# Kernel tuning notes

Measured on AMD Instinct MI355X. Metric: run time of the kernel, lower is better.

## Reference

```python
import jax, jax.numpy as jnp
import numpy as np

B = 512        # batch
TW = 45        # raw wav token length
C = 512        # n_embd
H = 8          # heads
L = 8          # decoder layers
V = 1000       # wav vocab
NLAB = 5       # label vocab
HID = 2048     # 4*C mlp hidden
OH = 768       # output head hidden
WIN, TRAIN = 30, 44
LN_EPS = 1e-5


def _build_mask(t):
    # triangular (strict upper) + sliding-window lower band, tiled 3x3 over segments
    m = np.triu(np.ones((TRAIN, TRAIN), dtype=bool), 1)
    for i in range(WIN, TRAIN):
        m[i, : i - WIN + 1] = True
    m = m[:t, :t]
    return jnp.asarray(np.tile(m, (3, 3)))  # [3t, 3t], True = masked


def setup_inputs() -> dict:
    key = jax.random.key(0)
    ks = iter(jax.random.split(key, 64))

    def rn(shape, s=0.02):
        return jax.random.normal(next(ks), shape, jnp.float32) * s

    inp = {
        'label': jax.random.randint(next(ks), (B, 1), 0, NLAB),
        'wav1': jax.random.randint(next(ks), (B, TW), 0, V),
        'wav2': jax.random.randint(next(ks), (B, TW), 0, V),
        # embeddings
        'emb_label': rn((NLAB, C), 1.0),
        'emb_w1': rn((V, C), 1.0),
        'emb_w2': rn((V, C), 1.0),
        # per-layer stacked params (leading dim L) for lax.scan
        'ln1_g': jnp.ones((L, 3, C), jnp.float32),
        'ln1_b': jnp.zeros((L, 3, C), jnp.float32),
        'ln2_g': jnp.ones((L, 3, C), jnp.float32),
        'ln2_b': jnp.zeros((L, 3, C), jnp.float32),
        'Wq': rn((L, C, C)), 'bq': jnp.zeros((L, C), jnp.float32),
        'Wk': rn((L, C, C)), 'bk': jnp.zeros((L, C), jnp.float32),
        'Wv': rn((L, C, C)), 'bv': jnp.zeros((L, C), jnp.float32),
        'Wp': rn((L, C, C)), 'bp': jnp.zeros((L, C), jnp.float32),
        'W1': rn((L, C, HID)), 'b1': jnp.zeros((L, HID), jnp.float32),
        'W2': rn((L, HID, C)), 'b2': jnp.zeros((L, C), jnp.float32),
        # output heads
        'o1W1': rn((C, OH)), 'o1b1': jnp.zeros((OH,), jnp.float32),
        'o1W2': rn((OH, V)), 'o1b2': jnp.zeros((V,), jnp.float32),
        'o2W1': rn((C, OH)), 'o2b1': jnp.zeros((OH,), jnp.float32),
        'o2W2': rn((OH, V)), 'o2b2': jnp.zeros((V,), jnp.float32),
    }
    return inp


def _forward(label, wav1, wav2, emb_label, emb_w1, emb_w2,
             ln1_g, ln1_b, ln2_g, ln2_b, Wq, bq, Wk, bk, Wv, bv, Wp, bp,
             W1, b1, W2, b2, o1W1, o1b1, o1W2, o1b2, o2W1, o2b1, o2W2, o2b2):
    wav1_src, wav1_tgt = wav1[:, :-1], wav1[:, 1:]
    wav2_src, wav2_tgt = wav2[:, :-1], wav2[:, 1:]
    b, t = wav1_src.shape
    label_rep = jnp.broadcast_to(label, (b, t))

    feat = jnp.concatenate([emb_label[label_rep], emb_w1[wav1_src], emb_w2[wav2_src]], axis=1)  # [B,3t,C]
    mask = _build_mask(t)  # [3t,3t] bool
    hd = C // H

    def ln3(x, g, be):
        # three separate LayerNorms over the 3 equal segments
        xr = x.reshape(b, 3, t, C)
        mu = xr.mean(-1, keepdims=True)
        var = xr.var(-1, keepdims=True)
        xn = (xr - mu) * jax.lax.rsqrt(var + LN_EPS)
        return (xn * g[None, :, None, :] + be[None, :, None, :]).reshape(b, 3 * t, C)

    def layer(x, p):
        g1, be1, g2, be2, wq, bq_, wk, bk_, wv, bv_, wp, bp_, w1, b1_, w2, b2_ = p
        h = ln3(x, g1, be1)
        q = (h @ wq + bq_).reshape(b, 3 * t, H, hd).transpose(0, 2, 1, 3)
        k = (h @ wk + bk_).reshape(b, 3 * t, H, hd).transpose(0, 2, 1, 3)
        v = (h @ wv + bv_).reshape(b, 3 * t, H, hd).transpose(0, 2, 1, 3)
        att = jnp.einsum('bhqd,bhkd->bhqk', q, k) * (1.0 / np.sqrt(hd))
        att = jnp.where(mask[None, None], -jnp.inf, att)
        att = jax.nn.softmax(att, axis=-1)
        y = jnp.einsum('bhqk,bhkd->bhqd', att, v).transpose(0, 2, 1, 3).reshape(b, 3 * t, C)
        x = x + (y @ wp + bp_)
        h2 = ln3(x, g2, be2)
        m = jax.nn.gelu(h2 @ w1 + b1_, approximate=False) @ w2 + b2_
        return x + m, None

    params = (ln1_g, ln1_b, ln2_g, ln2_b, Wq, bq, Wk, bk, Wv, bv, Wp, bp, W1, b1, W2, b2)
    x, _ = jax.lax.scan(layer, feat, params)

    wav1_pred = (x[:, t:2 * t] @ o1W1 + o1b1) @ o1W2 + o1b2  # [B,t,V]
    wav2_pred = (x[:, 2 * t:] @ o2W1 + o2b1) @ o2W2 + o2b2

    def ce(logits, tgt):
        lp = jax.nn.log_softmax(logits.reshape(-1, V).astype(jnp.float32), axis=-1)
        return -jnp.mean(jnp.take_along_axis(lp, tgt.reshape(-1, 1), axis=1))

    return ce(wav1_pred, wav1_tgt) + ce(wav2_pred, wav2_tgt)


def reference(label, wav1, wav2, emb_label, emb_w1, emb_w2,
              ln1_g, ln1_b, ln2_g, ln2_b, Wq, bq, Wk, bk, Wv, bv, Wp, bp,
              W1, b1, W2, b2, o1W1, o1b1, o1W2, o1b2, o2W1, o2b1, o2W2, o2b2):
    return _forward(label, wav1, wav2, emb_label, emb_w1, emb_w2,
                    ln1_g, ln1_b, ln2_g, ln2_b, Wq, bq, Wk, bk, Wv, bv, Wp, bp,
                    W1, b1, W2, b2, o1W1, o1b1, o1W2, o1b2, o2W1, o2b1, o2W2, o2b2)
```

## Files before the change

kernel.cpp:

```cpp
#include <hip/hip_runtime.h>

typedef __attribute__((ext_vector_type(4))) float f32x4;
typedef __attribute__((ext_vector_type(8))) __bf16 bf16x8;
typedef __attribute__((ext_vector_type(8))) unsigned short u16x8;

#define NB 512
#define TT 44
#define S3 132
#define CC 512
#define NH 8
#define NL 8
#define NV 1000
#define VP 1024
#define HID 2048
#define OH 768
#define WINW 30
#define QKVN 1536

#define HROWS (NB*TT)

#define WT_OFF   0ull
#define WC1T_OFF 50331648ull
#define WC2T_OFF 51380224ull
#define BC1_OFF  52428800ull
#define BC2_OFF  52432896ull
#define BQKV_OFF 52436992ull
#define LOSS_OFF 52486144ull
#define FIXED_SZ 52666368ull
#define PER_CHB  811008ull

#define LAYER_WELEMS 3145728ull

__device__ inline bf16x8 zero8() { u16x8 z = (u16x8)0; return *(bf16x8*)&z; }

#define STAGE(bufi, k0) do { \
  _Pragma("unroll") \
  for (int i_ = 0; i_ < 2; ++i_) { \
    int off_ = wid * 2048 + i_ * 1024; \
    int myoff_ = off_ + lane * 16; \
    int row_ = myoff_ >> 6; \
    int colb_ = myoff_ & 63; \
    const char* sa_ = (const char*)(A + (arow + row_) * (size_t)K + (k0)) + colb_; \
    const char* sb_ = (const char*)(Bt + (brow + row_) * (size_t)K + (k0)) + colb_; \
    __builtin_amdgcn_global_load_lds((const __attribute__((address_space(1))) void*)sa_, \
        (__attribute__((address_space(3))) void*)((char*)&As[bufi][0] + off_), 16, 0, 0); \
    __builtin_amdgcn_global_load_lds((const __attribute__((address_space(1))) void*)sb_, \
        (__attribute__((address_space(3))) void*)((char*)&Bs[bufi][0] + off_), 16, 0, 0); \
  } \
} while (0)

template<int EPI, typename OutT, typename ResT>
__global__ __launch_bounds__(256) void gemm_bt(
    const __bf16* __restrict__ A, const __bf16* __restrict__ Bt,
    const float* __restrict__ bias, const ResT* __restrict__ resid,
    OutT* __restrict__ C, int M, int N, int K)
{
    __shared__ __bf16 As[2][128 * 32];
    __shared__ __bf16 Bs[2][128 * 32];
    const int tid = threadIdx.x, lane = tid & 63, wid = tid >> 6;
    const int l15 = lane & 15, lk = lane >> 4;
    const int wr = wid >> 1, wc = wid & 1;

    const int nwg = gridDim.x * gridDim.y;
    const int orig = blockIdx.y * gridDim.x + blockIdx.x;
    const int qq = nwg >> 3, rr = nwg & 7;
    const int xcd = orig & 7, loc = orig >> 3;
    const int wg = (xcd < rr ? xcd * (qq + 1) : rr * (qq + 1) + (xcd - rr) * qq) + loc;
    const int bn = wg % gridDim.x, bm = wg / gridDim.x;

    f32x4 acc[4][4];
#pragma unroll
    for (int i = 0; i < 4; ++i)
#pragma unroll
        for (int j = 0; j < 4; ++j) acc[i][j] = (f32x4)0.f;

    const size_t arow = (size_t)bm * 128;
    const size_t brow = (size_t)bn * 128;
    const int KT = K >> 5;

    STAGE(0, 0);
    __syncthreads();

    int buf = 0;
    for (int kt = 0; kt < KT; ++kt) {
        if (kt + 1 < KT) STAGE(buf ^ 1, (kt + 1) << 5);
        bf16x8 af[4], bfv[4];
#pragma unroll
        for (int mi = 0; mi < 4; ++mi) af[mi] = *(const bf16x8*)&As[buf][(wr * 64 + mi * 16 + l15) * 32 + lk * 8];
#pragma unroll
        for (int ni = 0; ni < 4; ++ni) bfv[ni] = *(const bf16x8*)&Bs[buf][(wc * 64 + ni * 16 + l15) * 32 + lk * 8];
#pragma unroll
        for (int mi = 0; mi < 4; ++mi)
#pragma unroll
            for (int ni = 0; ni < 4; ++ni)
                acc[mi][ni] = __builtin_amdgcn_mfma_f32_16x16x32_bf16(af[mi], bfv[ni], acc[mi][ni], 0, 0, 0);
        __syncthreads();
        buf ^= 1;
    }

#pragma unroll
    for (int mi = 0; mi < 4; ++mi) {
#pragma unroll
        for (int ni = 0; ni < 4; ++ni) {
            int n = bn * 128 + wc * 64 + ni * 16 + l15;
            float bv = (EPI & 1) ? bias[n] : 0.f;
#pragma unroll
            for (int r = 0; r < 4; ++r) {
                int m = bm * 128 + wr * 64 + mi * 16 + lk * 4 + r;
                float v = acc[mi][ni][r] + bv;
                if (EPI & 2) v += (float)resid[(size_t)m * N + n];
                if (EPI & 4) v = 0.5f * v * (1.f + erff(v * 0.70710678118f));
                C[(size_t)m * N + n] = (OutT)v;
            }
        }
    }
}

__global__ __launch_bounds__(256) void attn_k(const __bf16* __restrict__ QKV,
                                              __bf16* __restrict__ Y)
{
    __shared__ __bf16 Kl[144 * 64];
    __shared__ __bf16 Ql[144 * 64];
    __shared__ __bf16 Vt[64 * 160];
    __shared__ __bf16 Pl[4][16 * 160];
    const int tid = threadIdx.x, lane = tid & 63, wid = tid >> 6;
    const int l15 = lane & 15, lk = lane >> 4;
    const int bh = blockIdx.x;
    const int b = bh >> 3, h = bh & 7;
    const size_t base = ((size_t)b * S3) * QKVN + h * 64;
    const size_t ybase = ((size_t)b * S3) * CC + h * 64;

    for (int i = tid; i < 144 * 64 / 8; i += 256) {
        int s = i >> 3, c = (i & 7) * 8;
        bf16x8 kv = zero8(), qv = zero8();
        if (s < S3) {
            qv = *(const bf16x8*)(QKV + base + (size_t)s * QKVN + c);
            kv = *(const bf16x8*)(QKV + base + (size_t)s * QKVN + 512 + c);
        }
        *(bf16x8*)&Kl[s * 64 + c] = kv;
        *(bf16x8*)&Ql[s * 64 + c] = qv;
    }
    for (int i = tid; i < 160 * 64; i += 256) {
        int s = i >> 6, d = i & 63;
        float v = 0.f;
        if (s < S3) v = (float)QKV[base + (size_t)s * QKVN + 1024 + d];
        Vt[d * 160 + s] = (__bf16)v;
    }
    for (int i = lane; i < 16 * 16; i += 64) {
        int r = i >> 4, c = i & 15;
        Pl[wid][r * 160 + 144 + c] = (__bf16)0.f;
    }
    __syncthreads();

    for (int qb = wid; qb < 9; qb += 4) {
        f32x4 st[9];
#pragma unroll
        for (int kt = 0; kt < 9; ++kt) {
            f32x4 a = (f32x4)0.f;
#pragma unroll
            for (int ks = 0; ks < 2; ++ks) {
                bf16x8 kf = *(const bf16x8*)&Kl[(kt * 16 + l15) * 64 + ks * 32 + lk * 8];
                bf16x8 qf = *(const bf16x8*)&Ql[(qb * 16 + l15) * 64 + ks * 32 + lk * 8];
                a = __builtin_amdgcn_mfma_f32_16x16x32_bf16(kf, qf, a, 0, 0, 0);
            }
            st[kt] = a;
        }
        int sq = qb * 16 + l15;
        int sqe = sq < S3 ? sq : (S3 - 1);
        int qm = sqe % TT;
        float mx = -1e30f;
#pragma unroll
        for (int kt = 0; kt < 9; ++kt)
#pragma unroll
            for (int r = 0; r < 4; ++r) {
                int sk = kt * 16 + lk * 4 + r;
                float sv = st[kt][r] * 0.125f;
                int kk = sk % TT;
                bool msk = (sk >= S3) || (kk > qm) || (qm >= WINW && kk <= qm - WINW);
                sv = msk ? -INFINITY : sv;
                st[kt][r] = sv;
                mx = fmaxf(mx, sv);
            }
        mx = fmaxf(mx, __shfl_xor(mx, 16));
        mx = fmaxf(mx, __shfl_xor(mx, 32));
        float sum = 0.f;
#pragma unroll
        for (int kt = 0; kt < 9; ++kt)
#pragma unroll
            for (int r = 0; r < 4; ++r) {
                float p = expf(st[kt][r] - mx);
                st[kt][r] = p;
                sum += p;
            }
        sum += __shfl_xor(sum, 16);
        sum += __shfl_xor(sum, 32);
        float inv = 1.f / sum;
#pragma unroll
        for (int kt = 0; kt < 9; ++kt)
#pragma unroll
            for (int r = 0; r < 4; ++r)
                Pl[wid][l15 * 160 + kt * 16 + lk * 4 + r] = (__bf16)(st[kt][r] * inv);
#pragma unroll
        for (int dt = 0; dt < 4; ++dt) {
            f32x4 o = (f32x4)0.f;
#pragma unroll
            for (int ks = 0; ks < 5; ++ks) {
                bf16x8 pa = *(const bf16x8*)&Pl[wid][l15 * 160 + ks * 32 + lk * 8];
                bf16x8 vb = *(const bf16x8*)&Vt[(dt * 16 + l15) * 160 + ks * 32 + lk * 8];
                o = __builtin_amdgcn_mfma_f32_16x16x32_bf16(pa, vb, o, 0, 0, 0);
            }
            int d = dt * 16 + l15;
#pragma unroll
            for (int r = 0; r < 4; ++r) {
                int sqr = qb * 16 + lk * 4 + r;
                if (sqr < S3) Y[ybase + (size_t)sqr * CC + d] = (__bf16)o[r];
            }
        }
    }
}

__global__ __launch_bounds__(256) void ln3_k(const __bf16* __restrict__ X,
                                             const float* __restrict__ g,
                                             const float* __restrict__ be,
                                             __bf16* __restrict__ Hb)
{
    int row = blockIdx.x * 4 + (threadIdx.x >> 6);
    int lane = threadIdx.x & 63;
    int seg = (row % S3) / TT;
    bf16x8 xv = *(const bf16x8*)(X + (size_t)row * CC + lane * 8);
    float vv[8];
    float s = 0.f, ss = 0.f;
#pragma unroll
    for (int j = 0; j < 8; ++j) { vv[j] = (float)xv[j]; s += vv[j]; ss += vv[j] * vv[j]; }
#pragma unroll
    for (int o = 32; o; o >>= 1) { s += __shfl_xor(s, o); ss += __shfl_xor(ss, o); }
    float mu = s * (1.f / CC);
    float var = ss * (1.f / CC) - mu * mu;
    float rs = rsqrtf(var + 1e-5f);
    const float* gp = g + seg * CC + lane * 8;
    const float* bp = be + seg * CC + lane * 8;
    __bf16* op = Hb + (size_t)row * CC + lane * 8;
#pragma unroll
    for (int j = 0; j < 8; ++j) op[j] = (__bf16)((vv[j] - mu) * rs * gp[j] + bp[j]);
}

__global__ __launch_bounds__(128) void embed_k(const int* __restrict__ label,
                                               const int* __restrict__ wav1,
                                               const int* __restrict__ wav2,
                                               const float* __restrict__ el,
                                               const float* __restrict__ e1,
                                               const float* __restrict__ e2,
                                               __bf16* __restrict__ X, int b0)
{
    int row = blockIdx.x;
    int b = b0 + row / S3, p = row % S3;
    int seg = p / TT, pos = p % TT;
    int idx; const float* src;
    if (seg == 0) { idx = label[b]; src = el; }
    else if (seg == 1) { idx = wav1[b * 45 + pos]; src = e1; }
    else { idx = wav2[b * 45 + pos]; src = e2; }
    float4 v = *((const float4*)(src + (size_t)idx * CC) + threadIdx.x);
    __bf16* dst = X + (size_t)row * CC + threadIdx.x * 4;
    dst[0] = (__bf16)v.x; dst[1] = (__bf16)v.y; dst[2] = (__bf16)v.z; dst[3] = (__bf16)v.w;
}

__global__ void transpose_cast(const float* __restrict__ in, __bf16* __restrict__ out,
                               int R, int Cin, int Np, long long inStride, long long outStride)
{
    __shared__ float t[32][33];
    in += (size_t)blockIdx.z * inStride;
    out += (size_t)blockIdx.z * outStride;
    int r0 = blockIdx.x * 32, c0 = blockIdx.y * 32;
    int tx = threadIdx.x, ty = threadIdx.y;
#pragma unroll
    for (int k2 = 0; k2 < 4; ++k2) {
        int r = r0 + ty + k2 * 8, c = c0 + tx;
        t[ty + k2 * 8][tx] = (r < R && c < Cin) ? in[(size_t)r * Cin + c] : 0.f;
    }
    __syncthreads();
#pragma unroll
    for (int k2 = 0; k2 < 4; ++k2) {
        int c = c0 + ty + k2 * 8, r = r0 + tx;
        if (c < Np && r < R) out[(size_t)c * R + r] = (__bf16)t[tx][ty + k2 * 8];
    }
}

__global__ void cast_k(const float* __restrict__ in, __bf16* __restrict__ out, int n)
{
    int i = blockIdx.x * 256 + threadIdx.x;
    if (i < n) out[i] = (__bf16)in[i];
}

__global__ void build_bqkv(const float* __restrict__ bq, const float* __restrict__ bk,
                           const float* __restrict__ bv, float* __restrict__ out)
{
    int i = blockIdx.x * 256 + threadIdx.x;
    if (i >= NL * QKVN) return;
    int l = i / QKVN, c = i % QKVN;
    float v = (c < 512) ? bq[l * 512 + c] : (c < 1024 ? bk[l * 512 + c - 512] : bv[l * 512 + c - 1024]);
    out[i] = v;
}

__global__ __launch_bounds__(128) void gather_cast(const __bf16* __restrict__ X,
                                                   __bf16* __restrict__ out, int segoff)
{
    int row = blockIdx.x;
    int b = row / TT, s2 = row % TT;
    const uint2* src = (const uint2*)(X + ((size_t)b * S3 + segoff + s2) * CC) + threadIdx.x;
    uint2* dst = (uint2*)(out + (size_t)row * CC) + threadIdx.x;
    *dst = *src;
}

__global__ void combo_bias(const float* __restrict__ b1, const float* __restrict__ W2,
                           const float* __restrict__ b2, float* __restrict__ out)
{
    int v = blockIdx.x * 256 + threadIdx.x;
    if (v >= VP) return;
    float s = 0.f;
    if (v < NV) {
        s = b2[v];
        for (int o = 0; o < OH; ++o) s += b1[o] * W2[o * NV + v];
    }
    out[v] = s;
}

__global__ __launch_bounds__(256) void ce_k(const float* __restrict__ logits,
                                            const int* __restrict__ wav,
                                            float* __restrict__ loss)
{
    int row = blockIdx.x * 4 + (threadIdx.x >> 6);
    int lane = threadIdx.x & 63;
    const float* lg = logits + (size_t)row * VP;
    int b = row / TT, s2 = row % TT;
    int tgt = wav[b * 45 + s2 + 1];
    float m = -1e30f;
    for (int i = lane; i < NV; i += 64) m = fmaxf(m, lg[i]);
#pragma unroll
    for (int o = 32; o; o >>= 1) m = fmaxf(m, __shfl_xor(m, o));
    float sum = 0.f;
    for (int i = lane; i < NV; i += 64) sum += expf(lg[i] - m);
#pragma unroll
    for (int o = 32; o; o >>= 1) sum += __shfl_xor(sum, o);
    if (lane == 0) loss[row] = m + logf(sum) - lg[tgt];
}

__global__ __launch_bounds__(256) void ce_sum(const float* __restrict__ loss, float* __restrict__ out)
{
    float s = 0.f;
    for (int i = threadIdx.x; i < 2 * HROWS; i += 256) s += loss[i];
#pragma unroll
    for (int o = 32; o; o >>= 1) s += __shfl_xor(s, o);
    __shared__ float w4[4];
    if ((threadIdx.x & 63) == 0) w4[threadIdx.x >> 6] = s;
    __syncthreads();
    if (threadIdx.x == 0) out[0] = (w4[0] + w4[1] + w4[2] + w4[3]) * (1.f / HROWS);
}

extern "C" void kernel_launch(void* const* d_in, const int* in_sizes, int n_in,
                              void* d_out, int out_size, void* d_ws, size_t ws_size,
                              hipStream_t stream)
{
    int chb;
    if      (ws_size >= FIXED_SZ + 512ull * PER_CHB) chb = 512;
    else if (ws_size >= FIXED_SZ + 256ull * PER_CHB) chb = 256;
    else if (ws_size >= FIXED_SZ + 128ull * PER_CHB) chb = 128;
    else return;
    const int nch = NB / chb;
    const int crows = chb * S3;
    const int chr = chb * TT;

    const int*   label = (const int*)d_in[0];
    const int*   wav1  = (const int*)d_in[1];
    const int*   wav2  = (const int*)d_in[2];
    const float* el    = (const float*)d_in[3];
    const float* e1    = (const float*)d_in[4];
    const float* e2    = (const float*)d_in[5];
    const float* ln1g  = (const float*)d_in[6];
    const float* ln1b  = (const float*)d_in[7];
    const float* ln2g  = (const float*)d_in[8];
    const float* ln2b  = (const float*)d_in[9];
    const float* Wq    = (const float*)d_in[10];
    const float* bq    = (const float*)d_in[11];
    const float* Wk    = (const float*)d_in[12];
    const float* bk    = (const float*)d_in[13];
    const float* Wv    = (const float*)d_in[14];
    const float* bv    = (const float*)d_in[15];
    const float* Wp    = (const float*)d_in[16];
    const float* bp    = (const float*)d_in[17];
    const float* W1    = (const float*)d_in[18];
    const float* b1    = (const float*)d_in[19];
    const float* W2    = (const float*)d_in[20];
    const float* b2    = (const float*)d_in[21];
    const float* o1W1  = (const float*)d_in[22];
    const float* o1b1  = (const float*)d_in[23];
    const float* o1W2  = (const float*)d_in[24];
    const float* o1b2  = (const float*)d_in[25];
    const float* o2W1  = (const float*)d_in[26];
    const float* o2b1  = (const float*)d_in[27];
    const float* o2W2  = (const float*)d_in[28];
    const float* o2b2  = (const float*)d_in[29];

    char* ws = (char*)d_ws;
    __bf16* WT    = (__bf16*)(ws + WT_OFF);
    __bf16* Wc1T  = (__bf16*)(ws + WC1T_OFF);
    __bf16* Wc2T  = (__bf16*)(ws + WC2T_OFF);
    float*  bc1   = (float*)(ws + BC1_OFF);
    float*  bc2   = (float*)(ws + BC2_OFF);
    float*  bqkv  = (float*)(ws + BQKV_OFF);
    float*  lossb = (float*)(ws + LOSS_OFF);
    __bf16* X     = (__bf16*)(ws + FIXED_SZ);
    __bf16* Hb    = (__bf16*)(ws + FIXED_SZ + (size_t)chb * 135168ull);
    char*   AR    = ws + FIXED_SZ + (size_t)chb * 270336ull;
    __bf16* o1W2T = (__bf16*)(AR + 0);
    __bf16* o2W2T = (__bf16*)(AR + 1572864);
    __bf16* o1W1b = (__bf16*)(AR + 3145728);
    __bf16* o2W1b = (__bf16*)(AR + 3932160);
    __bf16* qkvb   = (__bf16*)AR;
    __bf16* yb_    = Hb;
    __bf16* hidden = (__bf16*)AR;
    float*  logits = (float*)AR;
    __bf16* Xseg   = Hb;
    float*  outF   = (float*)d_out;

    dim3 tb(32, 8);
    transpose_cast<<<dim3(16, 16, NL), tb, 0, stream>>>(Wq, WT + 0,       CC, CC, CC, (long long)CC * CC, (long long)LAYER_WELEMS);
    transpose_cast<<<dim3(16, 16, NL), tb, 0, stream>>>(Wk, WT + 262144,  CC, CC, CC, (long long)CC * CC, (long long)LAYER_WELEMS);
    transpose_cast<<<dim3(16, 16, NL), tb, 0, stream>>>(Wv, WT + 524288,  CC, CC, CC, (long long)CC * CC, (long long)LAYER_WELEMS);
    transpose_cast<<<dim3(16, 16, NL), tb, 0, stream>>>(Wp, WT + 786432,  CC, CC, CC, (long long)CC * CC, (long long)LAYER_WELEMS);
    transpose_cast<<<dim3(16, 64, NL), tb, 0, stream>>>(W1, WT + 1048576, CC, HID, HID, (long long)CC * HID, (long long)LAYER_WELEMS);
    transpose_cast<<<dim3(64, 16, NL), tb, 0, stream>>>(W2, WT + 2097152, HID, CC, CC, (long long)HID * CC, (long long)LAYER_WELEMS);
    transpose_cast<<<dim3(24, 32, 1), tb, 0, stream>>>(o1W2, o1W2T, OH, NV, VP, 0, 0);
    transpose_cast<<<dim3(24, 32, 1), tb, 0, stream>>>(o2W2, o2W2T, OH, NV, VP, 0, 0);
    cast_k<<<(CC * OH + 255) / 256, 256, 0, stream>>>(o1W1, o1W1b, CC * OH);
    cast_k<<<(CC * OH + 255) / 256, 256, 0, stream>>>(o2W1, o2W1b, CC * OH);
    gemm_bt<0, __bf16, float><<<dim3(4, 8), 256, 0, stream>>>(o1W2T, o1W1b, nullptr, nullptr, Wc1T, VP, CC, OH);
    gemm_bt<0, __bf16, float><<<dim3(4, 8), 256, 0, stream>>>(o2W2T, o2W1b, nullptr, nullptr, Wc2T, VP, CC, OH);
    combo_bias<<<VP / 256, 256, 0, stream>>>(o1b1, o1W2, o1b2, bc1);
    combo_bias<<<VP / 256, 256, 0, stream>>>(o2b1, o2W2, o2b2, bc2);
    build_bqkv<<<(NL * QKVN + 255) / 256, 256, 0, stream>>>(bq, bk, bv, bqkv);

    for (int c = 0; c < nch; ++c) {
        int b0 = c * chb;
        embed_k<<<crows, 128, 0, stream>>>(label, wav1, wav2, el, e1, e2, X, b0);

        for (int l = 0; l < NL; ++l) {
            const __bf16* WqkvT = WT + (size_t)l * LAYER_WELEMS;
            const __bf16* WpT   = WT + (size_t)l * LAYER_WELEMS + 786432;
            const __bf16* W1T   = WT + (size_t)l * LAYER_WELEMS + 1048576;
            const __bf16* W2T   = WT + (size_t)l * LAYER_WELEMS + 2097152;

            ln3_k<<<crows / 4, 256, 0, stream>>>(X, ln1g + l * 3 * CC, ln1b + l * 3 * CC, Hb);
            gemm_bt<1, __bf16, float><<<dim3(QKVN / 128, crows / 128), 256, 0, stream>>>(Hb, WqkvT, bqkv + l * QKVN, nullptr, qkvb, crows, QKVN, CC);
            attn_k<<<chb * NH, 256, 0, stream>>>(qkvb, yb_);
            gemm_bt<3, __bf16, __bf16><<<dim3(4, crows / 128), 256, 0, stream>>>(yb_, WpT, bp + l * CC, X, X, crows, CC, CC);
            ln3_k<<<crows / 4, 256, 0, stream>>>(X, ln2g + l * 3 * CC, ln2b + l * 3 * CC, Hb);
            gemm_bt<5, __bf16, float><<<dim3(16, crows / 128), 256, 0, stream>>>(Hb, W1T, b1 + l * HID, nullptr, hidden, crows, HID, CC);
            gemm_bt<3, __bf16, __bf16><<<dim3(4, crows / 128), 256, 0, stream>>>(hidden, W2T, b2 + l * CC, X, X, crows, CC, HID);
        }

        gather_cast<<<chr, 128, 0, stream>>>(X, Xseg, TT);
        gemm_bt<1, float, float><<<dim3(VP / 128, chr / 128), 256, 0, stream>>>(Xseg, Wc1T, bc1, nullptr, logits, chr, VP, CC);
        ce_k<<<chr / 4, 256, 0, stream>>>(logits, wav1 + b0 * 45, lossb + c * chr);
        gather_cast<<<chr, 128, 0, stream>>>(X, Xseg, 2 * TT);
        gemm_bt<1, float, float><<<dim3(VP / 128, chr / 128), 256, 0, stream>>>(Xseg, Wc2T, bc2, nullptr, logits, chr, VP, CC);
        ce_k<<<chr / 4, 256, 0, stream>>>(logits, wav2 + b0 * 45, lossb + HROWS + c * chr);
    }

    ce_sum<<<1, 256, 0, stream>>>(lossb, outF);
}
```

Before: 8.235 ms.

## Triple-buffer GEMM LDS staging with partial vmcnt waits and XOR swizzle

Moves the bf16 GEMM from double to triple buffering. Tile loads are issued two k-steps ahead, and each iteration waits only until the oldest tile's loads land (vmcnt(4)) before the barrier, instead of a full sync. Global-to-LDS addresses and fragment reads get an XOR swizzle to cut LDS bank conflicts on the 64-byte rows. This costs more LDS per block, which may lower occupancy, and the waitcnt in inline asm relies on the compiler's instruction ordering.

```diff
diff --git a/kernel.cpp b/kernel.cpp
--- a/kernel.cpp
+++ b/kernel.cpp
@@ -33,15 +33,15 @@
 
 __device__ inline bf16x8 zero8() { u16x8 z = (u16x8)0; return *(bf16x8*)&z; }
 
-#define STAGE(bufi, k0) do { \
+#define STAGE(bufi, ktile) do { \
   _Pragma("unroll") \
   for (int i_ = 0; i_ < 2; ++i_) { \
     int off_ = wid * 2048 + i_ * 1024; \
     int myoff_ = off_ + lane * 16; \
     int row_ = myoff_ >> 6; \
-    int colb_ = myoff_ & 63; \
-    const char* sa_ = (const char*)(A + (arow + row_) * (size_t)K + (k0)) + colb_; \
-    const char* sb_ = (const char*)(Bt + (brow + row_) * (size_t)K + (k0)) + colb_; \
+    int colb_ = (myoff_ & 63) ^ ((row_ & 3) << 4); \
+    const char* sa_ = (const char*)(A + (arow + row_) * (size_t)K + ((ktile) << 5)) + colb_; \
+    const char* sb_ = (const char*)(Bt + (brow + row_) * (size_t)K + ((ktile) << 5)) + colb_; \
     __builtin_amdgcn_global_load_lds((const __attribute__((address_space(1))) void*)sa_, \
         (__attribute__((address_space(3))) void*)((char*)&As[bufi][0] + off_), 16, 0, 0); \
     __builtin_amdgcn_global_load_lds((const __attribute__((address_space(1))) void*)sb_, \
@@ -49,17 +49,21 @@
   } \
 } while (0)
 
+#define WAITBAR4 asm volatile("s_waitcnt vmcnt(4)\n\ts_barrier" ::: "memory")
+#define WAITBAR0 asm volatile("s_waitcnt vmcnt(0)\n\ts_barrier" ::: "memory")
+
 template<int EPI, typename OutT, typename ResT>
 __global__ __launch_bounds__(256) void gemm_bt(
     const __bf16* __restrict__ A, const __bf16* __restrict__ Bt,
     const float* __restrict__ bias, const ResT* __restrict__ resid,
     OutT* __restrict__ C, int M, int N, int K)
 {
-    __shared__ __bf16 As[2][128 * 32];
-    __shared__ __bf16 Bs[2][128 * 32];
+    __shared__ __bf16 As[3][128 * 32];
+    __shared__ __bf16 Bs[3][128 * 32];
     const int tid = threadIdx.x, lane = tid & 63, wid = tid >> 6;
     const int l15 = lane & 15, lk = lane >> 4;
     const int wr = wid >> 1, wc = wid & 1;
+    const int swz = l15 & 3;
 
     const int nwg = gridDim.x * gridDim.y;
     const int orig = blockIdx.y * gridDim.x + blockIdx.x;
@@ -79,23 +83,28 @@
     const int KT = K >> 5;
 
     STAGE(0, 0);
-    __syncthreads();
-
-    int buf = 0;
+    STAGE(1, 1);
+    WAITBAR4;
+
+    int cur = 0, stg = 2;
     for (int kt = 0; kt < KT; ++kt) {
-        if (kt + 1 < KT) STAGE(buf ^ 1, (kt + 1) << 5);
         bf16x8 af[4], bfv[4];
 #pragma unroll
-        for (int mi = 0; mi < 4; ++mi) af[mi] = *(const bf16x8*)&As[buf][(wr * 64 + mi * 16 + l15) * 32 + lk * 8];
-#pragma unroll
-        for (int ni = 0; ni < 4; ++ni) bfv[ni] = *(const bf16x8*)&Bs[buf][(wc * 64 + ni * 16 + l15) * 32 + lk * 8];
+        for (int mi = 0; mi < 4; ++mi)
+            af[mi] = *(const bf16x8*)&As[cur][(wr * 64 + mi * 16 + l15) * 32 + ((lk ^ swz) * 8)];
+#pragma unroll
+        for (int ni = 0; ni < 4; ++ni)
+            bfv[ni] = *(const bf16x8*)&Bs[cur][(wc * 64 + ni * 16 + l15) * 32 + ((lk ^ swz) * 8)];
+        bool more = (kt + 2 < KT);
+        if (more) STAGE(stg, kt + 2);
 #pragma unroll
         for (int mi = 0; mi < 4; ++mi)
 #pragma unroll
             for (int ni = 0; ni < 4; ++ni)
                 acc[mi][ni] = __builtin_amdgcn_mfma_f32_16x16x32_bf16(af[mi], bfv[ni], acc[mi][ni], 0, 0, 0);
-        __syncthreads();
-        buf ^= 1;
+        if (more) { WAITBAR4; } else { WAITBAR0; }
+        cur = (cur == 2) ? 0 : cur + 1;
+        stg = (stg == 2) ? 0 : stg + 1;
     }
 
 #pragma unroll
```

Result: faster. 7.506 ms (-8.9%).

## Replace GEMM with 256x256-tile, 4-stage pipelined, LDS-swizzled kernel

Applied to the files above, without the earlier changes.

The 128x128 double-buffered GEMM is replaced by a 512-thread kernel with 256x256 output tiles, a four-deep LDS ring filled three stages ahead, and an XOR swizzle on the LDS layout to reduce bank conflicts. It also uses explicit vmcnt waits in place of full syncthreads and raises wave priority around the MFMA block. All GEMM launches are resized for the new tile. The bigger tiles should improve data reuse and hide load latency, but they need 128KB of LDS per block and more accumulator registers. They also assume M, N and chunk rows divide by 256, which may not hold for every launch, for example when chr is not a multiple of 256.

```diff
diff --git a/kernel.cpp b/kernel.cpp
--- a/kernel.cpp
+++ b/kernel.cpp
@@ -33,33 +33,30 @@
 
 __device__ inline bf16x8 zero8() { u16x8 z = (u16x8)0; return *(bf16x8*)&z; }
 
-#define STAGE(bufi, k0) do { \
+#define ST_UNIT(LDSP, MATP, baserow, t) do { \
   _Pragma("unroll") \
-  for (int i_ = 0; i_ < 2; ++i_) { \
-    int off_ = wid * 2048 + i_ * 1024; \
-    int myoff_ = off_ + lane * 16; \
-    int row_ = myoff_ >> 6; \
-    int colb_ = myoff_ & 63; \
-    const char* sa_ = (const char*)(A + (arow + row_) * (size_t)K + (k0)) + colb_; \
-    const char* sb_ = (const char*)(Bt + (brow + row_) * (size_t)K + (k0)) + colb_; \
-    __builtin_amdgcn_global_load_lds((const __attribute__((address_space(1))) void*)sa_, \
-        (__attribute__((address_space(3))) void*)((char*)&As[bufi][0] + off_), 16, 0, 0); \
-    __builtin_amdgcn_global_load_lds((const __attribute__((address_space(1))) void*)sb_, \
-        (__attribute__((address_space(3))) void*)((char*)&Bs[bufi][0] + off_), 16, 0, 0); \
+  for (int j_ = 0; j_ < 2; ++j_) { \
+    int d_ = tid * 16 + j_ * 8192; \
+    int row_ = d_ >> 6; \
+    int c2_ = (d_ & 63) ^ ((row_ & 3) << 4); \
+    const char* src_ = (const char*)(MATP + ((baserow) + row_) * (size_t)K + ((size_t)(t) << 5)) + c2_; \
+    __builtin_amdgcn_global_load_lds((const __attribute__((address_space(1))) void*)src_, \
+        (__attribute__((address_space(3))) void*)((char*)(LDSP) + d_), 16, 0, 0); \
   } \
 } while (0)
 
 template<int EPI, typename OutT, typename ResT>
-__global__ __launch_bounds__(256) void gemm_bt(
+__global__ __launch_bounds__(512, 2) void gemm256(
     const __bf16* __restrict__ A, const __bf16* __restrict__ Bt,
     const float* __restrict__ bias, const ResT* __restrict__ resid,
     OutT* __restrict__ C, int M, int N, int K)
 {
-    __shared__ __bf16 As[2][128 * 32];
-    __shared__ __bf16 Bs[2][128 * 32];
+    __shared__ __bf16 As[4][256 * 32];
+    __shared__ __bf16 Bs[4][256 * 32];
     const int tid = threadIdx.x, lane = tid & 63, wid = tid >> 6;
     const int l15 = lane & 15, lk = lane >> 4;
-    const int wr = wid >> 1, wc = wid & 1;
+    const int wm = wid >> 2, wn = wid & 3;
+    const int swz = (l15 & 3) << 4;
 
     const int nwg = gridDim.x * gridDim.y;
     const int orig = blockIdx.y * gridDim.x + blockIdx.x;
@@ -68,45 +65,56 @@
     const int wg = (xcd < rr ? xcd * (qq + 1) : rr * (qq + 1) + (xcd - rr) * qq) + loc;
     const int bn = wg % gridDim.x, bm = wg / gridDim.x;
 
-    f32x4 acc[4][4];
-#pragma unroll
-    for (int i = 0; i < 4; ++i)
+    f32x4 acc[8][4];
+#pragma unroll
+    for (int i = 0; i < 8; ++i)
 #pragma unroll
         for (int j = 0; j < 4; ++j) acc[i][j] = (f32x4)0.f;
 
-    const size_t arow = (size_t)bm * 128;
-    const size_t brow = (size_t)bn * 128;
+    const size_t arow = (size_t)bm * 256;
+    const size_t brow = (size_t)bn * 256;
     const int KT = K >> 5;
 
-    STAGE(0, 0);
-    __syncthreads();
-
-    int buf = 0;
-    for (int kt = 0; kt < KT; ++kt) {
-        if (kt + 1 < KT) STAGE(buf ^ 1, (kt + 1) << 5);
-        bf16x8 af[4], bfv[4];
-#pragma unroll
-        for (int mi = 0; mi < 4; ++mi) af[mi] = *(const bf16x8*)&As[buf][(wr * 64 + mi * 16 + l15) * 32 + lk * 8];
-#pragma unroll
-        for (int ni = 0; ni < 4; ++ni) bfv[ni] = *(const bf16x8*)&Bs[buf][(wc * 64 + ni * 16 + l15) * 32 + lk * 8];
-#pragma unroll
-        for (int mi = 0; mi < 4; ++mi)
+    ST_UNIT(As[0], A, arow, 0); ST_UNIT(Bs[0], Bt, brow, 0);
+    ST_UNIT(As[1], A, arow, 1); ST_UNIT(Bs[1], Bt, brow, 1);
+    ST_UNIT(As[2], A, arow, 2); ST_UNIT(Bs[2], Bt, brow, 2);
+    asm volatile("s_waitcnt vmcnt(8)\n\ts_barrier" ::: "memory");
+
+    for (int t = 0; t < KT; ++t) {
+        const int buf = t & 3;
+        const int sb = (t + 3) & 3;
+        const bool more = (t + 3 < KT);
+        bf16x8 afr[8], bfr[4];
+#pragma unroll
+        for (int mi = 0; mi < 8; ++mi) {
+            int row = wm * 128 + mi * 16 + l15;
+            afr[mi] = *(const bf16x8*)((const char*)&As[buf][0] + ((row * 64 + lk * 16) ^ swz));
+        }
+#pragma unroll
+        for (int ni = 0; ni < 4; ++ni) {
+            int row = wn * 64 + ni * 16 + l15;
+            bfr[ni] = *(const bf16x8*)((const char*)&Bs[buf][0] + ((row * 64 + lk * 16) ^ swz));
+        }
+        if (more) { ST_UNIT(As[sb], A, arow, t + 3); ST_UNIT(Bs[sb], Bt, brow, t + 3); }
+        __builtin_amdgcn_s_setprio(1);
+#pragma unroll
+        for (int mi = 0; mi < 8; ++mi)
 #pragma unroll
             for (int ni = 0; ni < 4; ++ni)
-                acc[mi][ni] = __builtin_amdgcn_mfma_f32_16x16x32_bf16(af[mi], bfv[ni], acc[mi][ni], 0, 0, 0);
-        __syncthreads();
-        buf ^= 1;
-    }
-
-#pragma unroll
-    for (int mi = 0; mi < 4; ++mi) {
+                acc[mi][ni] = __builtin_amdgcn_mfma_f32_16x16x32_bf16(afr[mi], bfr[ni], acc[mi][ni], 0, 0, 0);
+        __builtin_amdgcn_s_setprio(0);
+        asm volatile("s_waitcnt vmcnt(4)\n\ts_barrier" ::: "memory");
+    }
+
+#pragma unroll
+    for (int mi = 0; mi < 8; ++mi) {
 #pragma unroll
         for (int ni = 0; ni < 4; ++ni) {
-            int n = bn * 128 + wc * 64 + ni * 16 + l15;
+            int n = bn * 256 + wn * 64 + ni * 16 + l15;
             float bv = (EPI & 1) ? bias[n] : 0.f;
 #pragma unroll
             for (int r = 0; r < 4; ++r) {
-                int m = bm * 128 + wr * 64 + mi * 16 + lk * 4 + r;
+                int m = bm * 256 + wm * 128 + mi * 16 + lk * 4 + r;
                 float v = acc[mi][ni][r] + bv;
                 if (EPI & 2) v += (float)resid[(size_t)m * N + n];
                 if (EPI & 4) v = 0.5f * v * (1.f + erff(v * 0.70710678118f));
@@ -433,8 +441,8 @@
     transpose_cast<<<dim3(24, 32, 1), tb, 0, stream>>>(o2W2, o2W2T, OH, NV, VP, 0, 0);
     cast_k<<<(CC * OH + 255) / 256, 256, 0, stream>>>(o1W1, o1W1b, CC * OH);
     cast_k<<<(CC * OH + 255) / 256, 256, 0, stream>>>(o2W1, o2W1b, CC * OH);
-    gemm_bt<0, __bf16, float><<<dim3(4, 8), 256, 0, stream>>>(o1W2T, o1W1b, nullptr, nullptr, Wc1T, VP, CC, OH);
-    gemm_bt<0, __bf16, float><<<dim3(4, 8), 256, 0, stream>>>(o2W2T, o2W1b, nullptr, nullptr, Wc2T, VP, CC, OH);
+    gemm256<0, __bf16, float><<<dim3(2, 4), 512, 0, stream>>>(o1W2T, o1W1b, nullptr, nullptr, Wc1T, VP, CC, OH);
+    gemm256<0, __bf16, float><<<dim3(2, 4), 512, 0, stream>>>(o2W2T, o2W1b, nullptr, nullptr, Wc2T, VP, CC, OH);
     combo_bias<<<VP / 256, 256, 0, stream>>>(o1b1, o1W2, o1b2, bc1);
     combo_bias<<<VP / 256, 256, 0, stream>>>(o2b1, o2W2, o2b2, bc2);
     build_bqkv<<<(NL * QKVN + 255) / 256, 256, 0, stream>>>(bq, bk, bv, bqkv);
@@ -450,19 +458,19 @@
             const __bf16* W2T   = WT + (size_t)l * LAYER_WELEMS + 2097152;
 
             ln3_k<<<crows / 4, 256, 0, stream>>>(X, ln1g + l * 3 * CC, ln1b + l * 3 * CC, Hb);
-            gemm_bt<1, __bf16, float><<<dim3(QKVN / 128, crows / 128), 256, 0, stream>>>(Hb, WqkvT, bqkv + l * QKVN, nullptr, qkvb, crows, QKVN, CC);
+            gemm256<1, __bf16, float><<<dim3(QKVN / 256, crows / 256), 512, 0, stream>>>(Hb, WqkvT, bqkv + l * QKVN, nullptr, qkvb, crows, QKVN, CC);
             attn_k<<<chb * NH, 256, 0, stream>>>(qkvb, yb_);
-            gemm_bt<3, __bf16, __bf16><<<dim3(4, crows / 128), 256, 0, stream>>>(yb_, WpT, bp + l * CC, X, X, crows, CC, CC);
+            gemm256<3, __bf16, __bf16><<<dim3(2, crows / 256), 512, 0, stream>>>(yb_, WpT, bp + l * CC, X, X, crows, CC, CC);
             ln3_k<<<crows / 4, 256, 0, stream>>>(X, ln2g + l * 3 * CC, ln2b + l * 3 * CC, Hb);
-            gemm_bt<5, __bf16, float><<<dim3(16, crows / 128), 256, 0, stream>>>(Hb, W1T, b1 + l * HID, nullptr, hidden, crows, HID, CC);
-            gemm_bt<3, __bf16, __bf16><<<dim3(4, crows / 128), 256, 0, stream>>>(hidden, W2T, b2 + l * CC, X, X, crows, CC, HID);
+            gemm256<5, __bf16, float><<<dim3(HID / 256, crows / 256), 512, 0, stream>>>(Hb, W1T, b1 + l * HID, nullptr, hidden, crows, HID, CC);
+            gemm256<3, __bf16, __bf16><<<dim3(2, crows / 256), 512, 0, stream>>>(hidden, W2T, b2 + l * CC, X, X, crows, CC, HID);
         }
 
         gather_cast<<<chr, 128, 0, stream>>>(X, Xseg, TT);
-        gemm_bt<1, float, float><<<dim3(VP / 128, chr / 128), 256, 0, stream>>>(Xseg, Wc1T, bc1, nullptr, logits, chr, VP, CC);
+        gemm256<1, float, float><<<dim3(VP / 256, chr / 256), 512, 0, stream>>>(Xseg, Wc1T, bc1, nullptr, logits, chr, VP, CC);
         ce_k<<<chr / 4, 256, 0, stream>>>(logits, wav1 + b0 * 45, lossb + c * chr);
         gather_cast<<<chr, 128, 0, stream>>>(X, Xseg, 2 * TT);
-        gemm_bt<1, float, float><<<dim3(VP / 128, chr / 128), 256, 0, stream>>>(Xseg, Wc2T, bc2, nullptr, logits, chr, VP, CC);
+        gemm256<1, float, float><<<dim3(VP / 256, chr / 256), 512, 0, stream>>>(Xseg, Wc2T, bc2, nullptr, logits, chr, VP, CC);
         ce_k<<<chr / 4, 256, 0, stream>>>(logits, wav2 + b0 * 45, lossb + HROWS + c * chr);
     }
 
```

Result: slower. 8.467 ms (+2.8%).
